# Performance work log

Measured on AMD Instinct MI355X. Metric: run time of the kernel, lower is better.

Reference implementation:

```python
import jax, jax.numpy as jnp
import numpy as np

HIDDEN = 512
NUM_HEADS = 8
HEAD_DIM = HIDDEN // NUM_HEADS


def setup_inputs() -> dict:
    key = jax.random.key(0)
    k1, k2 = jax.random.split(key)
    x = jax.random.normal(k1, (2, 2048, HIDDEN), dtype=jnp.float32)
    # torch Linear(h, 3h, bias=False): weight shape [3h, h], y = x @ W.T
    W_qkv = jax.random.normal(k2, (3 * HIDDEN, HIDDEN), dtype=jnp.float32) * (HIDDEN ** -0.5)
    return {"x": x, "W_qkv": W_qkv}


def reference(x, W_qkv):
    B, S, h = x.shape
    H, d = NUM_HEADS, HEAD_DIM
    temperature = (1.0 / d) ** 0.5  # sqrt(1/head_dim)
    qkv = x @ W_qkv.T  # [B, S, 3h]
    # Original chunks 3h into H pieces of size 3d (per-head interleaved QKV),
    # stacks on dim=1 -> [B, H, S, 3d], then splits into Q, K, V.
    qkv = qkv.reshape(B, S, H, 3 * d).transpose(0, 2, 1, 3)  # [B, H, S, 3d]
    q, k, v = jnp.split(qkv, 3, axis=-1)  # each [B, H, S, d]
    scores = jnp.einsum("bhqd,bhkd->bhqk", q * temperature, k)  # [B, H, S, S]
    # dropout is inference no-op; mask branch in original is a dead assignment
    w = jax.nn.softmax(scores, axis=-1)
    out = jnp.einsum("bhqk,bhkd->bhqd", w, v)  # [B, H, S, d]
    # torch.cat over heads on last dim == transpose back + merge heads
    return out.transpose(0, 2, 1, 3).reshape(B, S, h)
```

## Files before the change

kernel.cpp:

```cpp
#include <hip/hip_runtime.h>
#include <stdint.h>

#define HD 512
#define NH 8
#define DH 64
#define SEQ 2048
#define BATCH 2
#define M_TOTAL (BATCH*SEQ)
#define N_QKV (3*HD)
#define K_DIM HD

typedef short bf16x8 __attribute__((ext_vector_type(8)));
typedef float f32x4 __attribute__((ext_vector_type(4)));
typedef uint32_t u32x2 __attribute__((ext_vector_type(2)));
typedef uint32_t u32x4 __attribute__((ext_vector_type(4)));

#define QSCALE 0.18033688011112042f

__device__ __forceinline__ uint16_t f2bf(float f) {
  union { float f; uint32_t u; } v; v.f = f;
  uint32_t u = v.u;
  return (uint16_t)((u + 0x7FFFu + ((u >> 16) & 1u)) >> 16);
}

__device__ __forceinline__ void gload_lds16(const void* g, void* l) {
  __builtin_amdgcn_global_load_lds(
      (const __attribute__((address_space(1))) void*)g,
      (__attribute__((address_space(3))) void*)l,
      16, 0, 0);
}

__global__ void convert_all(const float* __restrict__ x, const float* __restrict__ W,
                            uint16_t* __restrict__ xb, uint16_t* __restrict__ Wb) {
  const int nx4 = M_TOTAL * K_DIM / 4;
  const int nw4 = N_QKV * K_DIM / 4;
  int i = blockIdx.x * 256 + threadIdx.x;
  const float* src; uint16_t* dst; int j;
  if (i < nx4) { src = x; dst = xb; j = i; }
  else { j = i - nx4; if (j >= nw4) return; src = W; dst = Wb; }
  float4 v = reinterpret_cast<const float4*>(src)[j];
  ushort4 o;
  o.x = f2bf(v.x); o.y = f2bf(v.y); o.z = f2bf(v.z); o.w = f2bf(v.w);
  reinterpret_cast<ushort4*>(dst)[j] = o;
}

#define BM 64
#define BN 128
#define BK 64
#define NKT (K_DIM / BK)

__global__ __launch_bounds__(256)
void qkv_gemm(const uint16_t* __restrict__ A,
              const uint16_t* __restrict__ Bw,
              uint16_t* __restrict__ C,
              uint16_t* __restrict__ Vt) {
  __shared__ __align__(16) uint16_t As[2][BM * BK];
  __shared__ __align__(16) uint16_t Bs[2][BN * BK];

  const int t = threadIdx.x;
  const int lane = t & 63;
  const int w = t >> 6;
  const int l15 = lane & 15, l4 = lane >> 4;

  const int nbx = gridDim.x;
  const int nwg = nbx * gridDim.y;
  const int cpx = nwg >> 3;
  int id = blockIdx.y * nbx + blockIdx.x;
  int wid = (id & 7) * cpx + (id >> 3);
  const int m0 = (wid / nbx) * BM;
  const int n0 = (wid % nbx) * BN;

  f32x4 acc[4][2] = {};

  auto stage = [&](int kt, int buf) {
#pragma unroll
    for (int i = 0; i < 2; ++i) {
      int idx = t + 256 * i;
      int row = idx >> 3, slot = idx & 7;
      int src = slot ^ (row & 7);
      gload_lds16(A + (size_t)(m0 + row) * K_DIM + kt * BK + src * 8,
                  (char*)As[buf] + idx * 16);
    }
#pragma unroll
    for (int i = 0; i < 4; ++i) {
      int idx = t + 256 * i;
      int row = idx >> 3, slot = idx & 7;
      int src = slot ^ (row & 7);
      gload_lds16(Bw + (size_t)(n0 + row) * K_DIM + kt * BK + src * 8,
                  (char*)Bs[buf] + idx * 16);
    }
  };

  stage(0, 0);
  for (int kt = 0; kt < NKT; ++kt) {
    __syncthreads();
    if (kt + 1 < NKT) stage(kt + 1, (kt + 1) & 1);
    const char* Ab = (const char*)As[kt & 1];
    const char* Bb = (const char*)Bs[kt & 1];
#pragma unroll
    for (int kk = 0; kk < 2; ++kk) {
      bf16x8 af[4], bf[2];
#pragma unroll
      for (int i = 0; i < 4; ++i) {
        int rowa = i * 16 + l15;
        int sa = (kk * 4 + l4) ^ (rowa & 7);
        af[i] = *reinterpret_cast<const bf16x8*>(Ab + rowa * 128 + sa * 16);
      }
#pragma unroll
      for (int j = 0; j < 2; ++j) {
        int rowb = w * 32 + j * 16 + l15;
        int sb = (kk * 4 + l4) ^ (rowb & 7);
        bf[j] = *reinterpret_cast<const bf16x8*>(Bb + rowb * 128 + sb * 16);
      }
#pragma unroll
      for (int i = 0; i < 4; ++i)
#pragma unroll
        for (int j = 0; j < 2; ++j)
          acc[i][j] = __builtin_amdgcn_mfma_f32_16x16x32_bf16(af[i], bf[j], acc[i][j], 0, 0, 0);
    }
  }

  const int colw = n0 + w * 32;
  const int cmod = colw % 192;
  const bool isv = (cmod >= 128);
  __syncthreads();

  if (isv) {
    char* tb = (char*)As + w * 4096;
#pragma unroll
    for (int i = 0; i < 4; ++i)
#pragma unroll
      for (int j = 0; j < 2; ++j) {
        uint32_t lo, hi;
        asm("v_cvt_pk_bf16_f32 %0, %1, %2" : "=v"(lo) : "v"(acc[i][j][0]), "v"(acc[i][j][1]));
        asm("v_cvt_pk_bf16_f32 %0, %1, %2" : "=v"(hi) : "v"(acc[i][j][2]), "v"(acc[i][j][3]));
        int dloc = j * 16 + l15;
        int slot_s = i * 2 + (l4 >> 1);
        int byteoff = dloc * 128 + ((slot_s ^ (dloc & 7)) * 16) + (l4 & 1) * 8;
        u32x2 pk; pk.x = lo; pk.y = hi;
        *reinterpret_cast<u32x2*>(tb + byteoff) = pk;
      }
    int h = colw / 192;
    int d0 = cmod - 128;
    int b = m0 >> 11;
    int sbase = m0 & (SEQ - 1);
    uint16_t* vbase = Vt + ((size_t)(b * NH + h) * DH + d0) * SEQ + sbase + (lane & 7) * 8;
#pragma unroll
    for (int p = 0; p < 4; ++p) {
      int dl = p * 8 + (lane >> 3);
      u32x4 rv = *reinterpret_cast<const u32x4*>(
          tb + dl * 128 + (((lane & 7) ^ (dl & 7)) * 16));
      *reinterpret_cast<u32x4*>(vbase + (size_t)dl * SEQ) = rv;
    }
  } else {
    float sc = ((cmod >> 6) == 0) ? QSCALE : 1.0f;
#pragma unroll
    for (int i = 0; i < 4; ++i) {
      int row = m0 + i * 16 + l4 * 4;
#pragma unroll
      for (int j = 0; j < 2; ++j) {
        int col = colw + j * 16 + l15;
#pragma unroll
        for (int jj = 0; jj < 4; ++jj)
          C[(size_t)(row + jj) * N_QKV + col] = f2bf(acc[i][j][jj] * sc);
      }
    }
  }
}

#define NT (SEQ / 64)

__global__ __launch_bounds__(256, 6)
void attn(const uint16_t* __restrict__ qkv, const uint16_t* __restrict__ VtG,
          float* __restrict__ Po,
          float2* __restrict__ Pml) {
  __shared__ __align__(16) uint16_t Kt[64 * 64];
  __shared__ __align__(16) uint16_t Vt[64 * 64];
  __shared__ __align__(16) uint16_t Pl[4][16 * 64];

  const int t = threadIdx.x;
  const int lane = t & 63;
  const int w = t >> 6;
  const int l15 = lane & 15, l4 = lane >> 4;
  const int bh = blockIdx.x;
  const int b = bh >> 3, h = bh & 7;
  const int qw = blockIdx.y * 64 + w * 16;
  const int half = blockIdx.z;
  const int tph = NT / gridDim.z;
  const int t0 = half * tph;

  bf16x8 qf[2];
  {
    const uint16_t* qp = qkv + (size_t)(b * SEQ + qw + l15) * N_QKV + h * 192;
#pragma unroll
    for (int kk = 0; kk < 2; ++kk)
      qf[kk] = *reinterpret_cast<const bf16x8*>(qp + kk * 32 + l4 * 8);
  }

  const uint16_t* kgbase = qkv + (size_t)b * SEQ * N_QKV + h * 192 + 64;
  const uint16_t* vgbase = VtG + (size_t)bh * DH * SEQ;

  u32x4 kreg[2], vreg[2];
  auto loadrv = [&](int ti) {
    int s0 = ti * 64;
#pragma unroll
    for (int i = 0; i < 2; ++i) {
      int idx = t + 256 * i;
      int row = idx >> 3, slot = idx & 7;
      kreg[i] = *reinterpret_cast<const u32x4*>(
          kgbase + (size_t)(s0 + row) * N_QKV + slot * 8);
      vreg[i] = *reinterpret_cast<const u32x4*>(
          vgbase + (size_t)row * SEQ + s0 + slot * 8);
    }
  };
  auto writelds = [&]() {
#pragma unroll
    for (int i = 0; i < 2; ++i) {
      int idx = t + 256 * i;
      int row = idx >> 3, slot = idx & 7;
      int off = row * 128 + ((slot ^ (row & 7)) * 16);
      *reinterpret_cast<u32x4*>((char*)Kt + off) = kreg[i];
      *reinterpret_cast<u32x4*>((char*)Vt + off) = vreg[i];
    }
  };

  f32x4 o[4] = {};
  float mrow = -1e30f, lrow = 0.0f;

  loadrv(t0);
  const char* Kb = (const char*)Kt;
  const char* Vb = (const char*)Vt;
  for (int rel = 0; rel < tph; ++rel) {
    __syncthreads();
    writelds();
    __syncthreads();
    if (rel + 1 < tph) loadrv(t0 + rel + 1);

    f32x4 s[4] = {};
    __builtin_amdgcn_s_setprio(1);
#pragma unroll
    for (int c = 0; c < 4; ++c) {
#pragma unroll
      for (int kk = 0; kk < 2; ++kk) {
        int row = c * 16 + l15;
        int sl = (kk * 4 + l4) ^ (row & 7);
        bf16x8 kf = *reinterpret_cast<const bf16x8*>(Kb + row * 128 + sl * 16);
        s[c] = __builtin_amdgcn_mfma_f32_16x16x32_bf16(kf, qf[kk], s[c], 0, 0, 0);
      }
    }
    __builtin_amdgcn_s_setprio(0);

    float vmax = s[0][0];
#pragma unroll
    for (int c = 0; c < 4; ++c)
#pragma unroll
      for (int jj = 0; jj < 4; ++jj) vmax = fmaxf(vmax, s[c][jj]);
    vmax = fmaxf(vmax, __shfl_xor(vmax, 16, 64));
    vmax = fmaxf(vmax, __shfl_xor(vmax, 32, 64));

    if (!__all(vmax - mrow <= 11.0f)) {
      float mn = fmaxf(mrow, vmax);
      float sc;
      float darg = mrow - mn;
      asm("v_exp_f32 %0, %1" : "=v"(sc) : "v"(darg));
      mrow = mn;
      float sr[4];
#pragma unroll
      for (int jj = 0; jj < 4; ++jj) sr[jj] = __shfl(sc, l4 * 4 + jj, 64);
#pragma unroll
      for (int f = 0; f < 4; ++f)
#pragma unroll
        for (int jj = 0; jj < 4; ++jj) o[f][jj] *= sr[jj];
      lrow *= sc;
    }

    float p[16];
#pragma unroll
    for (int c = 0; c < 4; ++c)
#pragma unroll
      for (int jj = 0; jj < 4; ++jj) {
        float arg = s[c][jj] - mrow;
        float e;
        asm("v_exp_f32 %0, %1" : "=v"(e) : "v"(arg));
        p[c * 4 + jj] = e;
      }
    float a0 = (p[0] + p[1]) + (p[2] + p[3]);
    float a1 = (p[4] + p[5]) + (p[6] + p[7]);
    float a2 = (p[8] + p[9]) + (p[10] + p[11]);
    float a3 = (p[12] + p[13]) + (p[14] + p[15]);
    float tsum = (a0 + a1) + (a2 + a3);
    tsum += __shfl_xor(tsum, 16, 64);
    tsum += __shfl_xor(tsum, 32, 64);
    lrow += tsum;

#pragma unroll
    for (int c = 0; c < 4; ++c) {
      uint32_t lo, hi;
      asm("v_cvt_pk_bf16_f32 %0, %1, %2" : "=v"(lo) : "v"(p[c * 4 + 0]), "v"(p[c * 4 + 1]));
      asm("v_cvt_pk_bf16_f32 %0, %1, %2" : "=v"(hi) : "v"(p[c * 4 + 2]), "v"(p[c * 4 + 3]));
      int slot = 2 * c + (l4 >> 1);
      int byteoff = l15 * 128 + ((slot ^ (l15 & 7)) * 16) + (l4 & 1) * 8;
      u32x2 pk; pk.x = lo; pk.y = hi;
      *reinterpret_cast<u32x2*>((char*)Pl[w] + byteoff) = pk;
    }

    __builtin_amdgcn_s_setprio(1);
#pragma unroll
    for (int kk = 0; kk < 2; ++kk) {
      int sp = (kk * 4 + l4) ^ (l15 & 7);
      bf16x8 pa = *reinterpret_cast<const bf16x8*>((const char*)Pl[w] + l15 * 128 + sp * 16);
#pragma unroll
      for (int f = 0; f < 4; ++f) {
        int d = f * 16 + l15;
        int sv = (kk * 4 + l4) ^ (d & 7);
        bf16x8 vf = *reinterpret_cast<const bf16x8*>(Vb + d * 128 + sv * 16);
        o[f] = __builtin_amdgcn_mfma_f32_16x16x32_bf16(pa, vf, o[f], 0, 0, 0);
      }
    }
    __builtin_amdgcn_s_setprio(0);
  }

  float* pob = Po + ((size_t)(half * 16 + bh) * SEQ) * DH;
#pragma unroll
  for (int f = 0; f < 4; ++f) {
    int d = f * 16 + l15;
#pragma unroll
    for (int jj = 0; jj < 4; ++jj) {
      int q = qw + l4 * 4 + jj;
      pob[(size_t)q * DH + d] = o[f][jj];
    }
  }
  if (lane < 16) {
    float2 ml; ml.x = mrow; ml.y = lrow;
    Pml[(size_t)(half * 16 + bh) * SEQ + qw + lane] = ml;
  }
}

__global__ __launch_bounds__(256)
void attn_combine(const float* __restrict__ Po, const float2* __restrict__ Pml,
                  float* __restrict__ out, int nsplit) {
  int idx = blockIdx.x * 256 + threadIdx.x;
  int d4 = idx & 15;
  int q = (idx >> 4) & (SEQ - 1);
  int bh = idx >> 15;
  int b = bh >> 3, h = bh & 7;

  float m = -1e30f;
  for (int s = 0; s < nsplit; ++s)
    m = fmaxf(m, Pml[(size_t)(s * 16 + bh) * SEQ + q].x);
  float den = 0.0f;
  f32x4 acc = {};
  for (int s = 0; s < nsplit; ++s) {
    float2 ml = Pml[(size_t)(s * 16 + bh) * SEQ + q];
    float a = exp2f(ml.x - m);
    den += ml.y * a;
    f32x4 ov = *reinterpret_cast<const f32x4*>(
        Po + ((size_t)(s * 16 + bh) * SEQ + q) * DH + d4 * 4);
#pragma unroll
    for (int i = 0; i < 4; ++i) acc[i] += ov[i] * a;
  }
  float rden = 1.0f / den;
  f32x4 res;
#pragma unroll
  for (int i = 0; i < 4; ++i) res[i] = acc[i] * rden;
  *reinterpret_cast<f32x4*>(out + ((size_t)(b * SEQ + q) * HD) + h * 64 + d4 * 4) = res;
}

extern "C" void kernel_launch(void* const* d_in, const int* in_sizes, int n_in,
                              void* d_out, int out_size, void* d_ws, size_t ws_size,
                              hipStream_t stream) {
  const float* x = (const float*)d_in[0];
  const float* Wq = (const float*)d_in[1];
  float* out = (float*)d_out;

  uint16_t* xb = (uint16_t*)d_ws;
  uint16_t* Wb = xb + (size_t)M_TOTAL * K_DIM;
  uint16_t* qkv = Wb + (size_t)N_QKV * K_DIM;
  uint16_t* vtg = qkv + (size_t)M_TOTAL * N_QKV;
  float* Po = (float*)(vtg + (size_t)16 * DH * SEQ);
  float2* Pml = (float2*)(Po + (size_t)4 * 16 * SEQ * DH);
  size_t base = (size_t)((char*)Po - (char*)d_ws);
  size_t per_split = (size_t)16 * SEQ * DH * 4 + (size_t)16 * SEQ * 8;
  int nsplit = 1;
  if (ws_size >= base + 4 * per_split) nsplit = 4;
  else if (ws_size >= base + 2 * per_split) nsplit = 2;

  convert_all<<<(M_TOTAL * K_DIM / 4 + N_QKV * K_DIM / 4 + 255) / 256, 256, 0, stream>>>(
      x, Wq, xb, Wb);

  dim3 g1(N_QKV / BN, M_TOTAL / BM);
  qkv_gemm<<<g1, 256, 0, stream>>>(xb, Wb, qkv, vtg);

  dim3 g2(BATCH * NH, SEQ / 64, nsplit);
  attn<<<g2, 256, 0, stream>>>(qkv, vtg, Po, Pml);

  attn_combine<<<(16 * SEQ * 16) / 256, 256, 0, stream>>>(Po, Pml, out, nsplit);
}
```

Baseline: 128.1 us.

## Double-buffer 32-wide KV tiles via direct global-to-LDS loads in attention

Shrinks the KV tile from 64 to 32 keys and double-buffers K and V in shared memory. Tiles are filled with direct global-to-LDS loads (gload_lds16) instead of register staging, which removes one barrier per iteration. The PV MFMA operands are swapped so the output accumulator is transposed; this drops the per-row rescale shuffles and allows vectorized f32x4 output stores. The smaller footprint raises the occupancy hint to 8 waves, at the cost of twice as many loop iterations and barriers.

```diff
diff --git a/kernel.cpp b/kernel.cpp
--- a/kernel.cpp
+++ b/kernel.cpp
@@ -168,15 +168,16 @@
   }
 }
 
-#define NT (SEQ / 64)
-
-__global__ __launch_bounds__(256, 6)
+#define KVB 32
+#define NT2 (SEQ / KVB)
+
+__global__ __launch_bounds__(256, 8)
 void attn(const uint16_t* __restrict__ qkv, const uint16_t* __restrict__ VtG,
           float* __restrict__ Po,
           float2* __restrict__ Pml) {
-  __shared__ __align__(16) uint16_t Kt[64 * 64];
-  __shared__ __align__(16) uint16_t Vt[64 * 64];
-  __shared__ __align__(16) uint16_t Pl[4][16 * 64];
+  __shared__ __align__(16) uint16_t Kt[2][KVB * 64];
+  __shared__ __align__(16) uint16_t Vt[2][DH * KVB];
+  __shared__ __align__(16) uint16_t Pl[4][16 * KVB];
 
   const int t = threadIdx.x;
   const int lane = t & 63;
@@ -186,7 +187,7 @@
   const int b = bh >> 3, h = bh & 7;
   const int qw = blockIdx.y * 64 + w * 16;
   const int half = blockIdx.z;
-  const int tph = NT / gridDim.z;
+  const int tph = NT2 / gridDim.z;
   const int t0 = half * tph;
 
   bf16x8 qf[2];
@@ -200,46 +201,36 @@
   const uint16_t* kgbase = qkv + (size_t)b * SEQ * N_QKV + h * 192 + 64;
   const uint16_t* vgbase = VtG + (size_t)bh * DH * SEQ;
 
-  u32x4 kreg[2], vreg[2];
-  auto loadrv = [&](int ti) {
-    int s0 = ti * 64;
-#pragma unroll
-    for (int i = 0; i < 2; ++i) {
-      int idx = t + 256 * i;
-      int row = idx >> 3, slot = idx & 7;
-      kreg[i] = *reinterpret_cast<const u32x4*>(
-          kgbase + (size_t)(s0 + row) * N_QKV + slot * 8);
-      vreg[i] = *reinterpret_cast<const u32x4*>(
-          vgbase + (size_t)row * SEQ + s0 + slot * 8);
+  auto stage = [&](int ti, int buf) {
+    int s0 = ti * KVB;
+    {
+      int row = t >> 3, slot = t & 7;
+      int src = slot ^ (row & 7);
+      gload_lds16(kgbase + (size_t)(s0 + row) * N_QKV + src * 8,
+                  (char*)Kt[buf] + t * 16);
+    }
+    {
+      int d = t >> 2, slot = t & 3;
+      int src = slot ^ (d & 3);
+      gload_lds16(vgbase + (size_t)d * SEQ + s0 + src * 8,
+                  (char*)Vt[buf] + t * 16);
     }
   };
-  auto writelds = [&]() {
-#pragma unroll
-    for (int i = 0; i < 2; ++i) {
-      int idx = t + 256 * i;
-      int row = idx >> 3, slot = idx & 7;
-      int off = row * 128 + ((slot ^ (row & 7)) * 16);
-      *reinterpret_cast<u32x4*>((char*)Kt + off) = kreg[i];
-      *reinterpret_cast<u32x4*>((char*)Vt + off) = vreg[i];
-    }
-  };
-
-  f32x4 o[4] = {};
+
+  f32x4 ot[4] = {};
   float mrow = -1e30f, lrow = 0.0f;
 
-  loadrv(t0);
-  const char* Kb = (const char*)Kt;
-  const char* Vb = (const char*)Vt;
+  stage(t0, 0);
   for (int rel = 0; rel < tph; ++rel) {
     __syncthreads();
-    writelds();
-    __syncthreads();
-    if (rel + 1 < tph) loadrv(t0 + rel + 1);
-
-    f32x4 s[4] = {};
+    if (rel + 1 < tph) stage(t0 + rel + 1, (rel + 1) & 1);
+    const char* Kb = (const char*)Kt[rel & 1];
+    const char* Vb = (const char*)Vt[rel & 1];
+
+    f32x4 s[2] = {};
     __builtin_amdgcn_s_setprio(1);
 #pragma unroll
-    for (int c = 0; c < 4; ++c) {
+    for (int c = 0; c < 2; ++c) {
 #pragma unroll
       for (int kk = 0; kk < 2; ++kk) {
         int row = c * 16 + l15;
@@ -252,7 +243,7 @@
 
     float vmax = s[0][0];
 #pragma unroll
-    for (int c = 0; c < 4; ++c)
+    for (int c = 0; c < 2; ++c)
 #pragma unroll
       for (int jj = 0; jj < 4; ++jj) vmax = fmaxf(vmax, s[c][jj]);
     vmax = fmaxf(vmax, __shfl_xor(vmax, 16, 64));
@@ -264,19 +255,16 @@
       float darg = mrow - mn;
       asm("v_exp_f32 %0, %1" : "=v"(sc) : "v"(darg));
       mrow = mn;
-      float sr[4];
-#pragma unroll
-      for (int jj = 0; jj < 4; ++jj) sr[jj] = __shfl(sc, l4 * 4 + jj, 64);
 #pragma unroll
       for (int f = 0; f < 4; ++f)
 #pragma unroll
-        for (int jj = 0; jj < 4; ++jj) o[f][jj] *= sr[jj];
+        for (int jj = 0; jj < 4; ++jj) ot[f][jj] *= sc;
       lrow *= sc;
     }
 
-    float p[16];
-#pragma unroll
-    for (int c = 0; c < 4; ++c)
+    float p[8];
+#pragma unroll
+    for (int c = 0; c < 2; ++c)
 #pragma unroll
       for (int jj = 0; jj < 4; ++jj) {
         float arg = s[c][jj] - mrow;
@@ -284,52 +272,39 @@
         asm("v_exp_f32 %0, %1" : "=v"(e) : "v"(arg));
         p[c * 4 + jj] = e;
       }
-    float a0 = (p[0] + p[1]) + (p[2] + p[3]);
-    float a1 = (p[4] + p[5]) + (p[6] + p[7]);
-    float a2 = (p[8] + p[9]) + (p[10] + p[11]);
-    float a3 = (p[12] + p[13]) + (p[14] + p[15]);
-    float tsum = (a0 + a1) + (a2 + a3);
+    float tsum = ((p[0] + p[1]) + (p[2] + p[3])) + ((p[4] + p[5]) + (p[6] + p[7]));
     tsum += __shfl_xor(tsum, 16, 64);
     tsum += __shfl_xor(tsum, 32, 64);
     lrow += tsum;
 
 #pragma unroll
-    for (int c = 0; c < 4; ++c) {
+    for (int c = 0; c < 2; ++c) {
       uint32_t lo, hi;
       asm("v_cvt_pk_bf16_f32 %0, %1, %2" : "=v"(lo) : "v"(p[c * 4 + 0]), "v"(p[c * 4 + 1]));
       asm("v_cvt_pk_bf16_f32 %0, %1, %2" : "=v"(hi) : "v"(p[c * 4 + 2]), "v"(p[c * 4 + 3]));
       int slot = 2 * c + (l4 >> 1);
-      int byteoff = l15 * 128 + ((slot ^ (l15 & 7)) * 16) + (l4 & 1) * 8;
+      int byteoff = l15 * 64 + ((slot ^ (l15 & 3)) * 16) + (l4 & 1) * 8;
       u32x2 pk; pk.x = lo; pk.y = hi;
       *reinterpret_cast<u32x2*>((char*)Pl[w] + byteoff) = pk;
     }
 
+    int sp = l4 ^ (l15 & 3);
+    bf16x8 pa = *reinterpret_cast<const bf16x8*>((const char*)Pl[w] + l15 * 64 + sp * 16);
     __builtin_amdgcn_s_setprio(1);
 #pragma unroll
-    for (int kk = 0; kk < 2; ++kk) {
-      int sp = (kk * 4 + l4) ^ (l15 & 7);
-      bf16x8 pa = *reinterpret_cast<const bf16x8*>((const char*)Pl[w] + l15 * 128 + sp * 16);
-#pragma unroll
-      for (int f = 0; f < 4; ++f) {
-        int d = f * 16 + l15;
-        int sv = (kk * 4 + l4) ^ (d & 7);
-        bf16x8 vf = *reinterpret_cast<const bf16x8*>(Vb + d * 128 + sv * 16);
-        o[f] = __builtin_amdgcn_mfma_f32_16x16x32_bf16(pa, vf, o[f], 0, 0, 0);
-      }
+    for (int f = 0; f < 4; ++f) {
+      int d = f * 16 + l15;
+      int sv = l4 ^ (d & 3);
+      bf16x8 vf = *reinterpret_cast<const bf16x8*>(Vb + d * 64 + sv * 16);
+      ot[f] = __builtin_amdgcn_mfma_f32_16x16x32_bf16(vf, pa, ot[f], 0, 0, 0);
     }
     __builtin_amdgcn_s_setprio(0);
   }
 
-  float* pob = Po + ((size_t)(half * 16 + bh) * SEQ) * DH;
-#pragma unroll
-  for (int f = 0; f < 4; ++f) {
-    int d = f * 16 + l15;
-#pragma unroll
-    for (int jj = 0; jj < 4; ++jj) {
-      int q = qw + l4 * 4 + jj;
-      pob[(size_t)q * DH + d] = o[f][jj];
-    }
-  }
+  float* pob = Po + ((size_t)(half * 16 + bh) * SEQ) * DH + (size_t)(qw + l15) * DH;
+#pragma unroll
+  for (int f = 0; f < 4; ++f)
+    *reinterpret_cast<f32x4*>(pob + f * 16 + l4 * 4) = ot[f];
   if (lane < 16) {
     float2 ml; ml.x = mrow; ml.y = lrow;
     Pml[(size_t)(half * 16 + bh) * SEQ + qw + lane] = ml;
```

New measurement: 121.4 us. 5.2% less time.

## Double-buffer K/V tiles via direct global-to-LDS loads and transpose PV output

Applied to the files above, without the earlier changes.

Replaces the register-staged K/V loads with direct global-to-LDS loads into double-buffered shared tiles, so each iteration needs one barrier instead of two. PV MFMA operands are swapped so the accumulator holds the transposed output, which removes the per-row shuffles during rescaling and enables vectorized f32x4 stores. The split-K factor drops from 4 to 2, and the occupancy hint in launch bounds is removed. Doubling LDS use and halving the split reduce parallelism and may lower occupancy. gload_lds16 is assumed to be defined in the hidden part of the file.

```diff
diff --git a/kernel.cpp b/kernel.cpp
--- a/kernel.cpp
+++ b/kernel.cpp
@@ -170,12 +170,12 @@
 
 #define NT (SEQ / 64)
 
-__global__ __launch_bounds__(256, 6)
+__global__ __launch_bounds__(256)
 void attn(const uint16_t* __restrict__ qkv, const uint16_t* __restrict__ VtG,
           float* __restrict__ Po,
           float2* __restrict__ Pml) {
-  __shared__ __align__(16) uint16_t Kt[64 * 64];
-  __shared__ __align__(16) uint16_t Vt[64 * 64];
+  __shared__ __align__(16) uint16_t Kt[2][64 * 64];
+  __shared__ __align__(16) uint16_t Vt[2][64 * 64];
   __shared__ __align__(16) uint16_t Pl[4][16 * 64];
 
   const int t = threadIdx.x;
@@ -200,41 +200,29 @@
   const uint16_t* kgbase = qkv + (size_t)b * SEQ * N_QKV + h * 192 + 64;
   const uint16_t* vgbase = VtG + (size_t)bh * DH * SEQ;
 
-  u32x4 kreg[2], vreg[2];
-  auto loadrv = [&](int ti) {
+  auto stage = [&](int ti, int buf) {
     int s0 = ti * 64;
 #pragma unroll
     for (int i = 0; i < 2; ++i) {
       int idx = t + 256 * i;
       int row = idx >> 3, slot = idx & 7;
-      kreg[i] = *reinterpret_cast<const u32x4*>(
-          kgbase + (size_t)(s0 + row) * N_QKV + slot * 8);
-      vreg[i] = *reinterpret_cast<const u32x4*>(
-          vgbase + (size_t)row * SEQ + s0 + slot * 8);
+      int src = slot ^ (row & 7);
+      gload_lds16(kgbase + (size_t)(s0 + row) * N_QKV + src * 8,
+                  (char*)Kt[buf] + idx * 16);
+      gload_lds16(vgbase + (size_t)row * SEQ + s0 + src * 8,
+                  (char*)Vt[buf] + idx * 16);
     }
   };
-  auto writelds = [&]() {
-#pragma unroll
-    for (int i = 0; i < 2; ++i) {
-      int idx = t + 256 * i;
-      int row = idx >> 3, slot = idx & 7;
-      int off = row * 128 + ((slot ^ (row & 7)) * 16);
-      *reinterpret_cast<u32x4*>((char*)Kt + off) = kreg[i];
-      *reinterpret_cast<u32x4*>((char*)Vt + off) = vreg[i];
-    }
-  };
-
-  f32x4 o[4] = {};
+
+  f32x4 ot[4] = {};
   float mrow = -1e30f, lrow = 0.0f;
 
-  loadrv(t0);
-  const char* Kb = (const char*)Kt;
-  const char* Vb = (const char*)Vt;
+  stage(t0, 0);
   for (int rel = 0; rel < tph; ++rel) {
     __syncthreads();
-    writelds();
-    __syncthreads();
-    if (rel + 1 < tph) loadrv(t0 + rel + 1);
+    if (rel + 1 < tph) stage(t0 + rel + 1, (rel + 1) & 1);
+    const char* Kb = (const char*)Kt[rel & 1];
+    const char* Vb = (const char*)Vt[rel & 1];
 
     f32x4 s[4] = {};
     __builtin_amdgcn_s_setprio(1);
@@ -264,13 +252,10 @@
       float darg = mrow - mn;
       asm("v_exp_f32 %0, %1" : "=v"(sc) : "v"(darg));
       mrow = mn;
-      float sr[4];
-#pragma unroll
-      for (int jj = 0; jj < 4; ++jj) sr[jj] = __shfl(sc, l4 * 4 + jj, 64);
 #pragma unroll
       for (int f = 0; f < 4; ++f)
 #pragma unroll
-        for (int jj = 0; jj < 4; ++jj) o[f][jj] *= sr[jj];
+        for (int jj = 0; jj < 4; ++jj) ot[f][jj] *= sc;
       lrow *= sc;
     }
 
@@ -314,22 +299,16 @@
         int d = f * 16 + l15;
         int sv = (kk * 4 + l4) ^ (d & 7);
         bf16x8 vf = *reinterpret_cast<const bf16x8*>(Vb + d * 128 + sv * 16);
-        o[f] = __builtin_amdgcn_mfma_f32_16x16x32_bf16(pa, vf, o[f], 0, 0, 0);
+        ot[f] = __builtin_amdgcn_mfma_f32_16x16x32_bf16(vf, pa, ot[f], 0, 0, 0);
       }
     }
     __builtin_amdgcn_s_setprio(0);
   }
 
-  float* pob = Po + ((size_t)(half * 16 + bh) * SEQ) * DH;
-#pragma unroll
-  for (int f = 0; f < 4; ++f) {
-    int d = f * 16 + l15;
-#pragma unroll
-    for (int jj = 0; jj < 4; ++jj) {
-      int q = qw + l4 * 4 + jj;
-      pob[(size_t)q * DH + d] = o[f][jj];
-    }
-  }
+  float* pob = Po + ((size_t)(half * 16 + bh) * SEQ) * DH + (size_t)(qw + l15) * DH;
+#pragma unroll
+  for (int f = 0; f < 4; ++f)
+    *reinterpret_cast<f32x4*>(pob + f * 16 + l4 * 4) = ot[f];
   if (lane < 16) {
     float2 ml; ml.x = mrow; ml.y = lrow;
     Pml[(size_t)(half * 16 + bh) * SEQ + qw + lane] = ml;
@@ -378,12 +357,10 @@
   uint16_t* qkv = Wb + (size_t)N_QKV * K_DIM;
   uint16_t* vtg = qkv + (size_t)M_TOTAL * N_QKV;
   float* Po = (float*)(vtg + (size_t)16 * DH * SEQ);
-  float2* Pml = (float2*)(Po + (size_t)4 * 16 * SEQ * DH);
+  float2* Pml = (float2*)(Po + (size_t)2 * 16 * SEQ * DH);
   size_t base = (size_t)((char*)Po - (char*)d_ws);
   size_t per_split = (size_t)16 * SEQ * DH * 4 + (size_t)16 * SEQ * 8;
-  int nsplit = 1;
-  if (ws_size >= base + 4 * per_split) nsplit = 4;
-  else if (ws_size >= base + 2 * per_split) nsplit = 2;
+  int nsplit = (ws_size >= base + 2 * per_split) ? 2 : 1;
 
   convert_all<<<(M_TOTAL * K_DIM / 4 + N_QKV * K_DIM / 4 + 255) / 256, 256, 0, stream>>>(
       x, Wq, xb, Wb);
```

Result: faster. 114.4 us (-10.7%).
